# Kernel optimization log

Measured on AMD Instinct MI355X. Metric: run time of the kernel, lower is better.

The kernel has to match this reference:

```python
import jax, jax.numpy as jnp
import numpy as np

TOP_K = 2  # config.num_active_experts


def setup_inputs() -> dict:
    key = jax.random.key(0)
    k1, k2, k3, k4 = jax.random.split(key, 4)
    B, S, D = 2, 2048, 1024
    E, W = 8, 1024  # 8 experts, each width 1024 -> total_expert_width = 8192
    x = jax.random.normal(k1, (B, S, D), dtype=jnp.float32)
    router_w = jax.random.normal(k2, (E, D), dtype=jnp.float32) * 0.02
    w1 = jax.random.normal(k3, (D, E * W), dtype=jnp.float32) * 0.02
    w2 = jax.random.normal(k4, (E * W, D), dtype=jnp.float32) * 0.02
    return {"x": x, "router_w": router_w, "w1": w1, "w2": w2}


def reference(x, router_w, w1, w2):
    B, S, D = x.shape
    E = router_w.shape[0]
    W = w1.shape[1] // E  # uniform expert width
    T = B * S
    xf = x.reshape(T, D)

    # Router: sigmoid gating, top-k, sum-normalized weights (norm_topk_prob)
    router_logits = jnp.einsum('td,ed->te', xf, router_w)
    router_probs = jax.nn.sigmoid(router_logits.astype(jnp.float32))
    top_w, sel = jax.lax.top_k(router_probs, TOP_K)          # [T,K]
    top_w = top_w / (top_w.sum(axis=-1, keepdims=True) + 1e-20)
    top_w = top_w.astype(x.dtype)

    # Expert MLPs: expert e uses w1[:, off_e:off_e+W], w2[off_e:off_e+W, :].
    # Uniform width -> single batched einsum over experts (same math as the
    # padded-gather / block-sparse SDD/DSD grouped GEMM pipeline).
    W1e = w1.reshape(D, E, W).transpose(1, 0, 2)             # [E,D,W]
    W2e = w2.reshape(E, W, D)                                # [E,W,D]
    h = jnp.einsum('td,edw->etw', xf, W1e)                   # up-proj
    a = jnp.square(jax.nn.relu(h))                           # relu_squared
    y = jnp.einsum('etw,ewd->etd', a, W2e)                   # down-proj

    # Weighted scatter-combine: combine_weights[t,e] = top_w if e selected else 0
    cw = jnp.zeros((T, E), dtype=x.dtype).at[jnp.arange(T)[:, None], sel].set(top_w)
    out = jnp.einsum('etd,te->td', y, cw)
    return out.reshape(B, S, D)
```

## Files before the change

kernel.cpp:

```cpp
#include <hip/hip_runtime.h>
#include <hip/hip_bf16.h>


#define T_TOKENS 4096
#define DD 1024
#define EE 8
#define WW 1024
#define CAP 1536
#define BM 128
#define BN 128
#define BK 64
#define MT (CAP / BM)
#define NT (WW / BN)
#define GEMM_BLOCKS (EE * MT * NT)
#define TR1_BLOCKS 512
#define TLD 132

typedef short bf16x8 __attribute__((ext_vector_type(8)));
typedef float f32x4 __attribute__((ext_vector_type(4)));

__device__ __forceinline__ void gload_lds16(const void* g, void* l) {
  __builtin_amdgcn_global_load_lds((__attribute__((address_space(1))) void*)(g),
                                   (__attribute__((address_space(3))) void*)(l),
                                   16, 0, 0);
}

__device__ __forceinline__ float bf2f(unsigned short u) {
  union { unsigned int i; float f; } v; v.i = (unsigned int)u << 16; return v.f;
}

__device__ __forceinline__ unsigned short f2bf_u(float f) {
  __hip_bfloat16 h = __float2bfloat16(f);
  union { __hip_bfloat16 h; unsigned short u; } c; c.h = h; return c.u;
}

__device__ __forceinline__ void transpose_tile_128(
    const float* __restrict__ src, long src_ld, long r0, long c0,
    unsigned short* __restrict__ dst, long dst_ld, unsigned short* lds)
{
  int tid = threadIdx.x;
  int cq = tid & 31;
  int rb = tid >> 5;
#pragma unroll
  for (int i = 0; i < 16; i++) {
    int r = rb + i * 8;
    f32x4 v = *(const f32x4*)(src + (r0 + r) * src_ld + c0 + cq * 4);
#pragma unroll
    for (int j = 0; j < 4; j++)
      lds[(cq * 4 + j) * TLD + r] = f2bf_u(v[j]);
  }
  __syncthreads();
#pragma unroll
  for (int it = 0; it < 8; it++) {
    int slot = it * 256 + tid;
    int c = slot >> 4;
    int m = slot & 15;
    const unsigned short* p = lds + (size_t)c * TLD + m * 8;
    uint2 lo = *(const uint2*)(p);
    uint2 hi = *(const uint2*)(p + 4);
    uint4 o; o.x = lo.x; o.y = lo.y; o.z = hi.x; o.w = hi.y;
    *(uint4*)(dst + (c0 + c) * dst_ld + r0 + m * 8) = o;
  }
}

__global__ __launch_bounds__(256) void pre_kernel(
    const float* __restrict__ w1, const float* __restrict__ x,
    const float* __restrict__ rw,
    __hip_bfloat16* __restrict__ w1t, __hip_bfloat16* __restrict__ xb,
    int* __restrict__ sel, float* __restrict__ wpair)
{
  __shared__ unsigned short lds_t[128 * TLD];
  int b = blockIdx.x;
  if (b < TR1_BLOCKS) {
    int e = b & 7;
    int t = b >> 3;
    int bn = e * 8 + (t >> 3);
    int bd = t & 7;
    transpose_tile_128(w1, EE * WW, (long)bd * 128, (long)bn * 128,
                       (unsigned short*)w1t, DD, lds_t);
  } else {
    int lane = threadIdx.x & 63;
    int wave = threadIdx.x >> 6;
    int t = (b - TR1_BLOCKS) * 4 + wave;
    const float* xrow = x + (size_t)t * DD;
    unsigned short* xbrow = (unsigned short*)xb + (size_t)t * DD;
    float acc[EE];
#pragma unroll
    for (int e = 0; e < EE; e++) acc[e] = 0.f;
#pragma unroll
    for (int i = 0; i < DD / 256; i++) {
      int d = lane * 4 + i * 256;
      f32x4 xv = *(const f32x4*)(xrow + d);
      union { unsigned short u[4]; ushort4 v; } pk;
#pragma unroll
      for (int j = 0; j < 4; j++) pk.u[j] = f2bf_u(xv[j]);
      *(ushort4*)(xbrow + d) = pk.v;
#pragma unroll
      for (int e = 0; e < EE; e++) {
        f32x4 rv = *(const f32x4*)(rw + e * DD + d);
        acc[e] += xv[0] * rv[0] + xv[1] * rv[1] + xv[2] * rv[2] + xv[3] * rv[3];
      }
    }
#pragma unroll
    for (int e = 0; e < EE; e++) {
#pragma unroll
      for (int off = 32; off > 0; off >>= 1)
        acc[e] += __shfl_down(acc[e], off, 64);
    }
    if (lane == 0) {
      float p[EE];
#pragma unroll
      for (int e = 0; e < EE; e++) p[e] = 1.f / (1.f + expf(-acc[e]));
      int e0 = 0; float b0 = p[0];
      for (int e = 1; e < EE; e++) if (p[e] > b0) { b0 = p[e]; e0 = e; }
      int e1 = -1; float b1 = -1.f;
      for (int e = 0; e < EE; e++) {
        if (e == e0) continue;
        if (p[e] > b1) { b1 = p[e]; e1 = e; }
      }
      float s = b0 + b1 + 1e-20f;
      sel[t] = e0 | (e1 << 8);
      wpair[2 * t]     = b0 / s;
      wpair[2 * t + 1] = b1 / s;
    }
  }
}

__global__ __launch_bounds__(1024) void lists_w2t_kernel(
    const int* __restrict__ sel, int* __restrict__ counts,
    int* __restrict__ idx, int* __restrict__ tslot,
    const float* __restrict__ w2, __hip_bfloat16* __restrict__ w2t)
{
  __shared__ __attribute__((aligned(16))) unsigned short lds_t[128 * TLD];
  __shared__ int lcnt[EE];
  int bid = blockIdx.x;
  int tid = threadIdx.x;
  if (bid == 0) {
    int lane = tid & 63;
    if (tid < EE) lcnt[tid] = 0;
    __syncthreads();
    unsigned long long lower = (1ull << lane) - 1;
#pragma unroll
    for (int j = 0; j < T_TOKENS / 1024; j++) {
      int t = j * 1024 + tid;
      int s = sel[t];
      int e0 = s & 0xff, e1 = (s >> 8) & 0xff;
      int slot0 = 0, slot1 = 0;
#pragma unroll
      for (int e = 0; e < EE; e++) {
        unsigned long long m0 = __ballot(e0 == e);
        unsigned long long m1 = __ballot(e1 == e);
        int c0 = __popcll(m0), c1 = __popcll(m1);
        int base = 0;
        if (lane == 0 && (c0 + c1) > 0) base = atomicAdd(&lcnt[e], c0 + c1);
        base = __shfl(base, 0, 64);
        if (e0 == e) slot0 = base + __popcll(m0 & lower);
        if (e1 == e) slot1 = base + c0 + __popcll(m1 & lower);
      }
      int p0 = e0 * CAP + slot0, p1 = e1 * CAP + slot1;
      idx[p0] = t; idx[p1] = t;
      tslot[2 * t] = p0; tslot[2 * t + 1] = p1;
    }
    __syncthreads();
    if (tid < EE) counts[tid] = lcnt[tid];
  } else {
    int e = bid & 7;
    int t2 = (bid - 1) >> 3;
    const float* src = w2 + (long)e * WW * DD;
    unsigned short* dst = (unsigned short*)(w2t + (long)e * DD * WW);
    long r0 = (long)(t2 >> 3) * 128;
    long c0 = (long)(t2 & 7) * 128;
    int cq = tid & 31;
    int row = tid >> 5;
#pragma unroll
    for (int i = 0; i < 4; i++) {
      int r = row + i * 32;
      f32x4 v = *(const f32x4*)(src + (r0 + r) * DD + c0 + cq * 4);
#pragma unroll
      for (int j = 0; j < 4; j++)
        lds_t[(cq * 4 + j) * TLD + r] = f2bf_u(v[j]);
    }
    __syncthreads();
#pragma unroll
    for (int it = 0; it < 2; it++) {
      int slot = it * 1024 + tid;
      int c = slot >> 4;
      int m = slot & 15;
      const unsigned short* p = lds_t + (size_t)c * TLD + m * 8;
      uint2 lo = *(const uint2*)(p);
      uint2 hi = *(const uint2*)(p + 4);
      uint4 o; o.x = lo.x; o.y = lo.y; o.z = hi.x; o.w = hi.y;
      *(uint4*)(dst + (c0 + c) * WW + r0 + m * 8) = o;
    }
  }
}

__global__ __launch_bounds__(256, 3) void gemm1_kernel(
    const __hip_bfloat16* __restrict__ xb, const __hip_bfloat16* __restrict__ w1t,
    const int* __restrict__ counts, const int* __restrict__ idx,
    __hip_bfloat16* __restrict__ act)
{
  __shared__ __attribute__((aligned(16))) char smem[32768];
  short* As = (short*)smem;
  short* Bs = (short*)(smem + 16384);
  int bid = blockIdx.x;
  int e = bid & 7;
  int i = bid >> 3;
  int mt = i >> 3, nt = i & 7;
  int n_e = counts[e];
  if (mt * BM >= n_e) return;

  int tid = threadIdx.x;
  int lane = tid & 63;
  int wave = __builtin_amdgcn_readfirstlane(tid >> 6);
  int wm = (wave >> 1) * 64, wn = (wave & 1) * 64;
  int m16 = lane & 15, qd = lane >> 4;

  const __hip_bfloat16* gA[4];
  const __hip_bfloat16* gB[4];
#pragma unroll
  for (int i2 = 0; i2 < 4; i2++) {
    int s = i2 * 256 + tid;
    int r = s >> 3;
    int q = (s & 7) ^ (r & 7);
    int rowA = mt * BM + r;
    int slot = rowA < n_e ? rowA : n_e - 1;
    int tok = idx[e * CAP + slot];
    gA[i2] = xb + (size_t)tok * DD + q * 8;
    gB[i2] = w1t + ((size_t)e * WW + nt * BN + r) * DD + q * 8;
  }
  short* ldsA[4];
  short* ldsB[4];
#pragma unroll
  for (int i2 = 0; i2 < 4; i2++) {
    ldsA[i2] = As + (i2 * 256 + wave * 64) * 8;
    ldsB[i2] = Bs + (i2 * 256 + wave * 64) * 8;
  }

  int aoff[4][2], boff[4][2];
#pragma unroll
  for (int mi = 0; mi < 4; mi++) {
    int r = wm + mi * 16 + m16;
#pragma unroll
    for (int h = 0; h < 2; h++)
      aoff[mi][h] = (r * 8 + ((qd + h * 4) ^ (r & 7))) * 8;
  }
#pragma unroll
  for (int ni = 0; ni < 4; ni++) {
    int r = wn + ni * 16 + m16;
#pragma unroll
    for (int h = 0; h < 2; h++)
      boff[ni][h] = (r * 8 + ((qd + h * 4) ^ (r & 7))) * 8;
  }

  f32x4 zero = {0.f, 0.f, 0.f, 0.f};
  f32x4 acc[4][4];
#pragma unroll
  for (int mi = 0; mi < 4; mi++)
#pragma unroll
    for (int ni = 0; ni < 4; ni++) acc[mi][ni] = zero;

  for (int k0 = 0; k0 < DD; k0 += BK) {
#pragma unroll
    for (int i2 = 0; i2 < 4; i2++) gload_lds16(gA[i2] + k0, ldsA[i2]);
#pragma unroll
    for (int i2 = 0; i2 < 4; i2++) gload_lds16(gB[i2] + k0, ldsB[i2]);
    __syncthreads();
#pragma unroll
    for (int h = 0; h < 2; h++) {
      bf16x8 af[4], bfr[4];
#pragma unroll
      for (int mi = 0; mi < 4; mi++) af[mi] = *(const bf16x8*)(As + aoff[mi][h]);
#pragma unroll
      for (int ni = 0; ni < 4; ni++) bfr[ni] = *(const bf16x8*)(Bs + boff[ni][h]);
#pragma unroll
      for (int mi = 0; mi < 4; mi++)
#pragma unroll
        for (int ni = 0; ni < 4; ni++)
          acc[mi][ni] = __builtin_amdgcn_mfma_f32_16x16x32_bf16(
              af[mi], bfr[ni], acc[mi][ni], 0, 0, 0);
    }
    __syncthreads();
  }

#pragma unroll
  for (int mi = 0; mi < 4; mi++) {
#pragma unroll
    for (int reg = 0; reg < 4; reg++) {
      int rowt = mt * BM + wm + mi * 16 + qd * 4 + reg;
      if (rowt < n_e) {
#pragma unroll
        for (int ni = 0; ni < 4; ni++) {
          float v = acc[mi][ni][reg];
          v = v > 0.f ? v * v : 0.f;
          int col = nt * BN + wn + ni * 16 + m16;
          act[((size_t)e * CAP + rowt) * WW + col] = __float2bfloat16(v);
        }
      }
    }
  }
}

__global__ __launch_bounds__(256, 3) void gemm2_kernel(
    const __hip_bfloat16* __restrict__ act, const __hip_bfloat16* __restrict__ w2t,
    const int* __restrict__ counts, __hip_bfloat16* __restrict__ y)
{
  __shared__ __attribute__((aligned(16))) char smem[32768];
  short* As = (short*)smem;
  short* Bs = (short*)(smem + 16384);
  int bid = blockIdx.x;
  int e = bid & 7;
  int i = bid >> 3;
  int mt = i >> 3, nt = i & 7;
  int n_e = counts[e];
  if (mt * BM >= n_e) return;

  int tid = threadIdx.x;
  int lane = tid & 63;
  int wave = __builtin_amdgcn_readfirstlane(tid >> 6);
  int wm = (wave >> 1) * 64, wn = (wave & 1) * 64;
  int m16 = lane & 15, qd = lane >> 4;

  const __hip_bfloat16* gA[4];
  const __hip_bfloat16* gB[4];
#pragma unroll
  for (int i2 = 0; i2 < 4; i2++) {
    int s = i2 * 256 + tid;
    int r = s >> 3;
    int q = (s & 7) ^ (r & 7);
    gA[i2] = act + ((size_t)e * CAP + mt * BM + r) * WW + q * 8;
    gB[i2] = w2t + ((size_t)e * DD + nt * BN + r) * WW + q * 8;
  }
  short* ldsA[4];
  short* ldsB[4];
#pragma unroll
  for (int i2 = 0; i2 < 4; i2++) {
    ldsA[i2] = As + (i2 * 256 + wave * 64) * 8;
    ldsB[i2] = Bs + (i2 * 256 + wave * 64) * 8;
  }

  int aoff[4][2], boff[4][2];
#pragma unroll
  for (int mi = 0; mi < 4; mi++) {
    int r = wm + mi * 16 + m16;
#pragma unroll
    for (int h = 0; h < 2; h++)
      aoff[mi][h] = (r * 8 + ((qd + h * 4) ^ (r & 7))) * 8;
  }
#pragma unroll
  for (int ni = 0; ni < 4; ni++) {
    int r = wn + ni * 16 + m16;
#pragma unroll
    for (int h = 0; h < 2; h++)
      boff[ni][h] = (r * 8 + ((qd + h * 4) ^ (r & 7))) * 8;
  }

  f32x4 zero = {0.f, 0.f, 0.f, 0.f};
  f32x4 acc[4][4];
#pragma unroll
  for (int mi = 0; mi < 4; mi++)
#pragma unroll
    for (int ni = 0; ni < 4; ni++) acc[mi][ni] = zero;

  for (int k0 = 0; k0 < WW; k0 += BK) {
#pragma unroll
    for (int i2 = 0; i2 < 4; i2++) gload_lds16(gA[i2] + k0, ldsA[i2]);
#pragma unroll
    for (int i2 = 0; i2 < 4; i2++) gload_lds16(gB[i2] + k0, ldsB[i2]);
    __syncthreads();
#pragma unroll
    for (int h = 0; h < 2; h++) {
      bf16x8 af[4], bfr[4];
#pragma unroll
      for (int mi = 0; mi < 4; mi++) af[mi] = *(const bf16x8*)(As + aoff[mi][h]);
#pragma unroll
      for (int ni = 0; ni < 4; ni++) bfr[ni] = *(const bf16x8*)(Bs + boff[ni][h]);
#pragma unroll
      for (int mi = 0; mi < 4; mi++)
#pragma unroll
        for (int ni = 0; ni < 4; ni++)
          acc[mi][ni] = __builtin_amdgcn_mfma_f32_16x16x32_bf16(
              af[mi], bfr[ni], acc[mi][ni], 0, 0, 0);
    }
    __syncthreads();
  }

#pragma unroll
  for (int mi = 0; mi < 4; mi++) {
#pragma unroll
    for (int reg = 0; reg < 4; reg++) {
      int slot = mt * BM + wm + mi * 16 + qd * 4 + reg;
      if (slot < n_e) {
#pragma unroll
        for (int ni = 0; ni < 4; ni++) {
          int col = nt * BN + wn + ni * 16 + m16;
          y[((size_t)e * CAP + slot) * DD + col] = __float2bfloat16(acc[mi][ni][reg]);
        }
      }
    }
  }
}

__global__ __launch_bounds__(256) void combine_kernel(
    const __hip_bfloat16* __restrict__ y, const int* __restrict__ tslot,
    const float* __restrict__ wpair, float* __restrict__ out)
{
  int c = threadIdx.x * 4;
  for (int t = blockIdx.x; t < T_TOKENS; t += 512) {
    int s0 = tslot[2 * t], s1 = tslot[2 * t + 1];
    float w0 = wpair[2 * t], w1 = wpair[2 * t + 1];
    const unsigned short* yu = (const unsigned short*)y;
    ushort4 a = *(const ushort4*)(yu + (size_t)s0 * DD + c);
    ushort4 bq = *(const ushort4*)(yu + (size_t)s1 * DD + c);
    f32x4 o;
    o[0] = w0 * bf2f(a.x) + w1 * bf2f(bq.x);
    o[1] = w0 * bf2f(a.y) + w1 * bf2f(bq.y);
    o[2] = w0 * bf2f(a.z) + w1 * bf2f(bq.z);
    o[3] = w0 * bf2f(a.w) + w1 * bf2f(bq.w);
    *(f32x4*)(out + (size_t)t * DD + c) = o;
  }
}

extern "C" void kernel_launch(void* const* d_in, const int* in_sizes, int n_in,
                              void* d_out, int out_size, void* d_ws, size_t ws_size,
                              hipStream_t stream)
{
  const float* x  = (const float*)d_in[0];
  const float* rw = (const float*)d_in[1];
  const float* w1 = (const float*)d_in[2];
  const float* w2 = (const float*)d_in[3];
  float* out = (float*)d_out;

  char* ws = (char*)d_ws;
  __hip_bfloat16* xb  = (__hip_bfloat16*)ws;  ws += (size_t)T_TOKENS * DD * 2;
  __hip_bfloat16* w1t = (__hip_bfloat16*)ws;  ws += (size_t)EE * WW * DD * 2;
  __hip_bfloat16* w2t = (__hip_bfloat16*)ws;  ws += (size_t)EE * DD * WW * 2;
  __hip_bfloat16* act = (__hip_bfloat16*)ws;  ws += (size_t)EE * CAP * WW * 2;
  __hip_bfloat16* y   = (__hip_bfloat16*)ws;  ws += (size_t)EE * CAP * DD * 2;
  int*   counts = (int*)ws;                   ws += 256;
  int*   idx    = (int*)ws;                   ws += (size_t)EE * CAP * 4;
  int*   sel    = (int*)ws;                   ws += (size_t)T_TOKENS * 4;
  int*   tslot  = (int*)ws;                   ws += (size_t)T_TOKENS * 8;
  float* wpair  = (float*)ws;                 ws += (size_t)T_TOKENS * 8;

  pre_kernel<<<TR1_BLOCKS + T_TOKENS / 4, 256, 0, stream>>>(
      w1, x, rw, w1t, xb, sel, wpair);
  lists_w2t_kernel<<<513, 1024, 0, stream>>>(sel, counts, idx, tslot, w2, w2t);
  gemm1_kernel<<<GEMM_BLOCKS, 256, 0, stream>>>(xb, w1t, counts, idx, act);
  gemm2_kernel<<<GEMM_BLOCKS, 256, 0, stream>>>(act, w2t, counts, y);
  combine_kernel<<<512, 256, 0, stream>>>(y, tslot, wpair, out);
}
```

Measured before the change: 189.2 us.

## Double-buffer LDS tiles in both expert GEMMs to overlap loads with MFMA

Both grouped GEMM kernels now use two 32 KB LDS buffers and prefetch the next K-tile with direct global-to-LDS loads while the current tile is being computed. Manual vmcnt waits and raw barriers replace the two __syncthreads per iteration. The goal is to hide global memory latency behind MFMA work. In exchange, LDS per block doubles and launch bounds drop from 3 to 2 blocks per CU, which lowers occupancy. The wait counts also rely on the compiler emitting exactly the expected number of outstanding loads.

```diff
diff --git a/kernel.cpp b/kernel.cpp
--- a/kernel.cpp
+++ b/kernel.cpp
@@ -195,14 +195,12 @@
   }
 }
 
-__global__ __launch_bounds__(256, 3) void gemm1_kernel(
+__global__ __launch_bounds__(256, 2) void gemm1_kernel(
     const __hip_bfloat16* __restrict__ xb, const __hip_bfloat16* __restrict__ w1t,
     const int* __restrict__ counts, const int* __restrict__ idx,
     __hip_bfloat16* __restrict__ act)
 {
-  __shared__ __attribute__((aligned(16))) char smem[32768];
-  short* As = (short*)smem;
-  short* Bs = (short*)(smem + 16384);
+  __shared__ __attribute__((aligned(16))) char smem[65536];
   int bid = blockIdx.x;
   int e = bid & 7;
   int i = bid >> 3;
@@ -229,13 +227,9 @@
     gA[i2] = xb + (size_t)tok * DD + q * 8;
     gB[i2] = w1t + ((size_t)e * WW + nt * BN + r) * DD + q * 8;
   }
-  short* ldsA[4];
-  short* ldsB[4];
-#pragma unroll
-  for (int i2 = 0; i2 < 4; i2++) {
-    ldsA[i2] = As + (i2 * 256 + wave * 64) * 8;
-    ldsB[i2] = Bs + (i2 * 256 + wave * 64) * 8;
-  }
+  int ldsOff[4];
+#pragma unroll
+  for (int i2 = 0; i2 < 4; i2++) ldsOff[i2] = (i2 * 256 + wave * 64) * 8;
 
   int aoff[4][2], boff[4][2];
 #pragma unroll
@@ -260,12 +254,29 @@
 #pragma unroll
     for (int ni = 0; ni < 4; ni++) acc[mi][ni] = zero;
 
-  for (int k0 = 0; k0 < DD; k0 += BK) {
-#pragma unroll
-    for (int i2 = 0; i2 < 4; i2++) gload_lds16(gA[i2] + k0, ldsA[i2]);
-#pragma unroll
-    for (int i2 = 0; i2 < 4; i2++) gload_lds16(gB[i2] + k0, ldsB[i2]);
-    __syncthreads();
+#pragma unroll
+  for (int i2 = 0; i2 < 4; i2++) {
+    gload_lds16(gA[i2], (short*)smem + ldsOff[i2]);
+    gload_lds16(gB[i2], (short*)(smem + 16384) + ldsOff[i2]);
+  }
+
+  int kk = 0;
+  for (int k0 = 0; k0 < DD; k0 += BK, kk ^= 1) {
+    if (k0 + BK < DD) {
+      char* nb = smem + (kk ^ 1) * 32768;
+#pragma unroll
+      for (int i2 = 0; i2 < 4; i2++) {
+        gload_lds16(gA[i2] + k0 + BK, (short*)nb + ldsOff[i2]);
+        gload_lds16(gB[i2] + k0 + BK, (short*)(nb + 16384) + ldsOff[i2]);
+      }
+      asm volatile("s_waitcnt vmcnt(8)" ::: "memory");
+    } else {
+      asm volatile("s_waitcnt vmcnt(0)" ::: "memory");
+    }
+    __builtin_amdgcn_s_barrier();
+    asm volatile("" ::: "memory");
+    short* As = (short*)(smem + kk * 32768);
+    short* Bs = (short*)(smem + kk * 32768 + 16384);
 #pragma unroll
     for (int h = 0; h < 2; h++) {
       bf16x8 af[4], bfr[4];
@@ -280,7 +291,9 @@
           acc[mi][ni] = __builtin_amdgcn_mfma_f32_16x16x32_bf16(
               af[mi], bfr[ni], acc[mi][ni], 0, 0, 0);
     }
-    __syncthreads();
+    asm volatile("" ::: "memory");
+    __builtin_amdgcn_s_barrier();
+    asm volatile("" ::: "memory");
   }
 
 #pragma unroll
@@ -301,13 +314,11 @@
   }
 }
 
-__global__ __launch_bounds__(256, 3) void gemm2_kernel(
+__global__ __launch_bounds__(256, 2) void gemm2_kernel(
     const __hip_bfloat16* __restrict__ act, const __hip_bfloat16* __restrict__ w2t,
     const int* __restrict__ counts, __hip_bfloat16* __restrict__ y)
 {
-  __shared__ __attribute__((aligned(16))) char smem[32768];
-  short* As = (short*)smem;
-  short* Bs = (short*)(smem + 16384);
+  __shared__ __attribute__((aligned(16))) char smem[65536];
   int bid = blockIdx.x;
   int e = bid & 7;
   int i = bid >> 3;
@@ -331,13 +342,9 @@
     gA[i2] = act + ((size_t)e * CAP + mt * BM + r) * WW + q * 8;
     gB[i2] = w2t + ((size_t)e * DD + nt * BN + r) * WW + q * 8;
   }
-  short* ldsA[4];
-  short* ldsB[4];
-#pragma unroll
-  for (int i2 = 0; i2 < 4; i2++) {
-    ldsA[i2] = As + (i2 * 256 + wave * 64) * 8;
-    ldsB[i2] = Bs + (i2 * 256 + wave * 64) * 8;
-  }
+  int ldsOff[4];
+#pragma unroll
+  for (int i2 = 0; i2 < 4; i2++) ldsOff[i2] = (i2 * 256 + wave * 64) * 8;
 
   int aoff[4][2], boff[4][2];
 #pragma unroll
@@ -362,12 +369,29 @@
 #pragma unroll
     for (int ni = 0; ni < 4; ni++) acc[mi][ni] = zero;
 
-  for (int k0 = 0; k0 < WW; k0 += BK) {
-#pragma unroll
-    for (int i2 = 0; i2 < 4; i2++) gload_lds16(gA[i2] + k0, ldsA[i2]);
-#pragma unroll
-    for (int i2 = 0; i2 < 4; i2++) gload_lds16(gB[i2] + k0, ldsB[i2]);
-    __syncthreads();
+#pragma unroll
+  for (int i2 = 0; i2 < 4; i2++) {
+    gload_lds16(gA[i2], (short*)smem + ldsOff[i2]);
+    gload_lds16(gB[i2], (short*)(smem + 16384) + ldsOff[i2]);
+  }
+
+  int kk = 0;
+  for (int k0 = 0; k0 < WW; k0 += BK, kk ^= 1) {
+    if (k0 + BK < WW) {
+      char* nb = smem + (kk ^ 1) * 32768;
+#pragma unroll
+      for (int i2 = 0; i2 < 4; i2++) {
+        gload_lds16(gA[i2] + k0 + BK, (short*)nb + ldsOff[i2]);
+        gload_lds16(gB[i2] + k0 + BK, (short*)(nb + 16384) + ldsOff[i2]);
+      }
+      asm volatile("s_waitcnt vmcnt(8)" ::: "memory");
+    } else {
+      asm volatile("s_waitcnt vmcnt(0)" ::: "memory");
+    }
+    __builtin_amdgcn_s_barrier();
+    asm volatile("" ::: "memory");
+    short* As = (short*)(smem + kk * 32768);
+    short* Bs = (short*)(smem + kk * 32768 + 16384);
 #pragma unroll
     for (int h = 0; h < 2; h++) {
       bf16x8 af[4], bfr[4];
@@ -382,7 +406,9 @@
           acc[mi][ni] = __builtin_amdgcn_mfma_f32_16x16x32_bf16(
               af[mi], bfr[ni], acc[mi][ni], 0, 0, 0);
     }
-    __syncthreads();
+    asm volatile("" ::: "memory");
+    __builtin_amdgcn_s_barrier();
+    asm volatile("" ::: "memory");
   }
 
 #pragma unroll
```

Result: no change. 192.6 us (+1.8%).
